# Kernel optimization log

Measured on AMD Instinct MI355X. Metric: run time of the kernel, lower is better.

The kernel has to match this reference:

```python
import jax, jax.numpy as jnp
import numpy as np

B = 4096
D = 1024
N = 100000
KS = (10000, 20000, 50000)


def _l2norm(x):
    # F.normalize(p=2, dim=1, eps=1e-12): x / max(||x||, eps)
    n = jnp.sqrt(jnp.sum(x * x, axis=1, keepdims=True))
    return x / jnp.maximum(n, 1e-12)


def setup_inputs() -> dict:
    key = jax.random.key(0)
    ks = jax.random.split(key, 16)
    inp = {}
    inp["anchor"] = jax.random.normal(ks[0], (B, D), jnp.float32)
    inp["index"] = jax.random.randint(ks[1], (B,), 0, N)
    for i, K in enumerate(KS):
        inp[f"inst2cluster{i}"] = jax.random.randint(ks[2 + i], (N,), 0, K)
        inp[f"centroids{i}"] = jax.random.normal(ks[5 + i], (K, D), jnp.float32)
        # density acts as a per-column temperature; keep it bounded away from 0
        inp[f"density{i}"] = jax.random.uniform(ks[8 + i], (K,), jnp.float32, 0.1, 1.0)
    return inp


def reference(anchor, centroids0, centroids1, centroids2,
              density0, density1, density2,
              index, inst2cluster0, inst2cluster1, inst2cluster2):
    Bn = anchor.shape[0]
    a = _l2norm(anchor)
    rows = jnp.arange(Bn)
    cols = jnp.arange(Bn - 1)
    # negatives[i, j] = sim[i, j + (j >= i)] -> row i without its diagonal entry
    neg_idx = cols[None, :] + (cols[None, :] >= rows[:, None])  # [B, B-1]

    scales = [(inst2cluster0, centroids0, density0),
              (inst2cluster1, centroids1, density1),
              (inst2cluster2, centroids2, density2)]
    n_scales = len(scales)

    loss = jnp.zeros(Bn, anchor.dtype)
    for i2c, cent, dens in scales:
        protos = _l2norm(cent)
        pos_id = i2c[index]                       # [B]
        sim = a @ protos[pos_id].T                # [B, B]
        pos = jnp.diagonal(sim)[:, None]          # [B, 1]
        neg = jnp.take_along_axis(sim, neg_idx, axis=1)  # [B, B-1]
        # torch broadcast: [B, B] / [B] divides column j by temp_proto[j]
        logits = jnp.concatenate([pos, neg], axis=1) / dens[pos_id][None, :]
        # CE with label 0, reduction='none'
        ce = jax.nn.logsumexp(logits, axis=1) - logits[:, 0]
        # faithful to the original: division by len(cluster_result) INSIDE the loop
        loss = (loss + ce) / n_scales
    return loss
```

## Files before the change

### kernel.cpp

```cpp
#include <hip/hip_runtime.h>

#define BB 4096
#define DD 1024
#define RTS (BB + 16)
#define BK 32
#define NT (DD / BK)

typedef float f32x4 __attribute__((ext_vector_type(4)));
typedef short bf16x8 __attribute__((ext_vector_type(8)));

__device__ __forceinline__ unsigned short f2bf(float f) {
  unsigned u = __float_as_uint(f);
  unsigned r = u + 0x7fffu + ((u >> 16) & 1u);
  return (unsigned short)(r >> 16);
}

__device__ __forceinline__ void async16(const void* g, void* l) {
  __builtin_amdgcn_global_load_lds(
      (const __attribute__((address_space(1))) void*)g,
      (__attribute__((address_space(3))) void*)l,
      16, 0, 0);
}

__global__ __launch_bounds__(256) void norm_anchor(const float* __restrict__ x,
                                                   unsigned short* __restrict__ y) {
  __shared__ float sred[4];
  const int row = blockIdx.x;
  const int tid = threadIdx.x;
  const float4 v = ((const float4*)(x + (size_t)row * DD))[tid];
  float ss = v.x * v.x + v.y * v.y + v.z * v.z + v.w * v.w;
#pragma unroll
  for (int off = 32; off > 0; off >>= 1) ss += __shfl_xor(ss, off, 64);
  if ((tid & 63) == 0) sred[tid >> 6] = ss;
  __syncthreads();
  const float tot = sred[0] + sred[1] + sred[2] + sred[3];
  const float inv = 1.0f / fmaxf(sqrtf(tot), 1e-12f);
  ushort4 o;
  o.x = f2bf(v.x * inv);
  o.y = f2bf(v.y * inv);
  o.z = f2bf(v.z * inv);
  o.w = f2bf(v.w * inv);
  ((ushort4*)(y + (size_t)row * DD))[tid] = o;
}

__global__ __launch_bounds__(256) void gather_norm(
    const int* __restrict__ index,
    const int* __restrict__ i2c0, const int* __restrict__ i2c1, const int* __restrict__ i2c2,
    const float* __restrict__ c0, const float* __restrict__ c1, const float* __restrict__ c2,
    const float* __restrict__ d0, const float* __restrict__ d1, const float* __restrict__ d2,
    unsigned short* __restrict__ p16, float* __restrict__ rt,
    float* __restrict__ rowacc) {
  __shared__ float sred[4];
  const int j = blockIdx.x;
  const int s = blockIdx.y;
  const int tid = threadIdx.x;
  const int* i2c = (s == 0) ? i2c0 : (s == 1) ? i2c1 : i2c2;
  const float* cent = (s == 0) ? c0 : (s == 1) ? c1 : c2;
  const float* dens = (s == 0) ? d0 : (s == 1) ? d1 : d2;
  const int pid = i2c[index[j]];
  const float4 v = ((const float4*)(cent + (size_t)pid * DD))[tid];
  float ss = v.x * v.x + v.y * v.y + v.z * v.z + v.w * v.w;
#pragma unroll
  for (int off = 32; off > 0; off >>= 1) ss += __shfl_xor(ss, off, 64);
  if ((tid & 63) == 0) sred[tid >> 6] = ss;
  __syncthreads();
  const float tot = sred[0] + sred[1] + sred[2] + sred[3];
  const float inv = 1.0f / fmaxf(sqrtf(tot), 1e-12f);
  unsigned short* out = p16 + ((size_t)s * BB + j) * DD;
  ushort4 o;
  o.x = f2bf(v.x * inv);
  o.y = f2bf(v.y * inv);
  o.z = f2bf(v.z * inv);
  o.w = f2bf(v.w * inv);
  ((ushort4*)out)[tid] = o;
  if (tid == 0) rt[(size_t)s * RTS + j] = 1.0f / dens[pid];
  if (tid == 1) rowacc[(size_t)s * BB + j] = 0.0f;
}

__global__ __launch_bounds__(512, 2) void gemm_ce_fused(const unsigned short* __restrict__ A,
                                                        const unsigned short* __restrict__ P,
                                                        const float* __restrict__ rt,
                                                        float* __restrict__ rowacc,
                                                        float* __restrict__ diag) {
  __shared__ __align__(16) unsigned short smem[4][2][8192];
  __shared__ float rsum[256][4];
  const int tid = threadIdx.x;
  const int lane = tid & 63;
  const int wave = tid >> 6;
  const int wm = wave >> 2;
  const int wn = wave & 3;
  const int m0 = blockIdx.y * 256;
  const int n0 = blockIdx.x * 256;
  const int s = blockIdx.z;
  const unsigned short* Bm = P + (size_t)s * BB * DD;
  const float* rt_s = rt + (size_t)s * RTS;

  const int row_l = lane >> 2;
  const int col_e = (((lane & 3) ^ ((row_l >> 1) & 3)) << 3);
  const int SA = wave * 2;
  const unsigned short* pA0 = A + (size_t)(m0 + SA * 16 + row_l) * DD + col_e;
  const unsigned short* pA1 = pA0 + (size_t)16 * DD;
  const unsigned short* pB0 = Bm + (size_t)(n0 + SA * 16 + row_l) * DD + col_e;
  const unsigned short* pB1 = pB0 + (size_t)16 * DD;

#pragma unroll
  for (int tt = 0; tt < 3; ++tt) {
    async16(pA0 + tt * BK, &smem[tt][0][SA * 512]);
    async16(pA1 + tt * BK, &smem[tt][0][(SA + 1) * 512]);
    async16(pB0 + tt * BK, &smem[tt][1][SA * 512]);
    async16(pB1 + tt * BK, &smem[tt][1][(SA + 1) * 512]);
  }
  const unsigned short* qA0 = pA0 + 3 * BK;
  const unsigned short* qA1 = pA1 + 3 * BK;
  const unsigned short* qB0 = pB0 + 3 * BK;
  const unsigned short* qB1 = pB1 + 3 * BK;

  const int fr = lane & 15;
  const int fq = lane >> 4;
  const int aoff = fr * 32 + ((fq ^ ((fr >> 1) & 3)) << 3);

  f32x4 acc[8][4];
#pragma unroll
  for (int mi = 0; mi < 8; ++mi)
#pragma unroll
    for (int ni = 0; ni < 4; ++ni) acc[mi][ni] = (f32x4){0.f, 0.f, 0.f, 0.f};

  for (int t = 0; t < NT; ++t) {
    const int bt = t & 3;
    const int bs = (t + 3) & 3;
    const bool stg = (t + 3 < NT);
    if (t < NT - 2)        asm volatile("s_waitcnt vmcnt(8)" ::: "memory");
    else if (t == NT - 2)  asm volatile("s_waitcnt vmcnt(4)" ::: "memory");
    else                   asm volatile("s_waitcnt vmcnt(0)" ::: "memory");
    __builtin_amdgcn_s_barrier();
    asm volatile("" ::: "memory");

    const unsigned short* la = &smem[bt][0][0];
    const unsigned short* lb = &smem[bt][1][0];

    if (stg) {
      async16(qA0, &smem[bs][0][SA * 512]);
      async16(qB0, &smem[bs][1][SA * 512]);
    }
    bf16x8 af[4], bv[4];
#pragma unroll
    for (int i = 0; i < 4; ++i) af[i] = *(const bf16x8*)&la[(wm * 8 + i) * 512 + aoff];
#pragma unroll
    for (int i = 0; i < 4; ++i) bv[i] = *(const bf16x8*)&lb[(wn * 4 + i) * 512 + aoff];
    __builtin_amdgcn_s_barrier();
    __builtin_amdgcn_s_setprio(1);
#pragma unroll
    for (int mi = 0; mi < 4; ++mi)
#pragma unroll
      for (int ni = 0; ni < 4; ++ni)
        acc[mi][ni] = __builtin_amdgcn_mfma_f32_16x16x32_bf16(af[mi], bv[ni], acc[mi][ni], 0, 0, 0);
    __builtin_amdgcn_s_setprio(0);
    __builtin_amdgcn_s_barrier();

    if (stg) {
      async16(qA1, &smem[bs][0][(SA + 1) * 512]);
      async16(qB1, &smem[bs][1][(SA + 1) * 512]);
      qA0 += BK; qA1 += BK; qB0 += BK; qB1 += BK;
    }
#pragma unroll
    for (int i = 0; i < 4; ++i) af[i] = *(const bf16x8*)&la[(wm * 8 + 4 + i) * 512 + aoff];
    __builtin_amdgcn_s_barrier();
    __builtin_amdgcn_s_setprio(1);
#pragma unroll
    for (int mi = 0; mi < 4; ++mi)
#pragma unroll
      for (int ni = 0; ni < 4; ++ni)
        acc[4 + mi][ni] = __builtin_amdgcn_mfma_f32_16x16x32_bf16(af[mi], bv[ni], acc[4 + mi][ni], 0, 0, 0);
    __builtin_amdgcn_s_setprio(0);
  }

  const int cm = fq * 4;
  const float rt0 = rt_s[0];
  float rtc[4], rtp[4];
#pragma unroll
  for (int ni = 0; ni < 4; ++ni) {
    const int col = n0 + wn * 64 + ni * 16 + fr;
    rtc[ni] = rt_s[col];
    rtp[ni] = rt_s[col + 1];
  }
#pragma unroll
  for (int mi = 0; mi < 8; ++mi) {
#pragma unroll
    for (int r = 0; r < 4; ++r) {
      const int rowi = m0 + wm * 128 + mi * 16 + cm + r;
      float esum = 0.f;
#pragma unroll
      for (int ni = 0; ni < 4; ++ni) {
        const int col = n0 + wn * 64 + ni * 16 + fr;
        const float v = acc[mi][ni][r];
        const float rr = (col == rowi) ? rt0 : ((col < rowi) ? rtp[ni] : rtc[ni]);
        const float l = v * rr;
        if (col == rowi) diag[(size_t)s * BB + rowi] = l;
        esum += __expf(l);
      }
#pragma unroll
      for (int off = 1; off < 16; off <<= 1) esum += __shfl_xor(esum, off, 64);
      if (fr == 0) rsum[wm * 128 + mi * 16 + cm + r][wn] = esum;
    }
  }
  __syncthreads();
  if (tid < 256) {
    const float v = rsum[tid][0] + rsum[tid][1] + rsum[tid][2] + rsum[tid][3];
    atomicAdd(&rowacc[(size_t)s * BB + m0 + tid], v);
  }
}

__global__ __launch_bounds__(256) void finish(const float* __restrict__ rowacc,
                                              const float* __restrict__ diag,
                                              float* __restrict__ out) {
  const int i = blockIdx.x * 256 + threadIdx.x;
  const float ce0 = logf(rowacc[i]) - diag[i];
  const float ce1 = logf(rowacc[BB + i]) - diag[BB + i];
  const float ce2 = logf(rowacc[2 * BB + i]) - diag[2 * BB + i];
  out[i] = ce0 * (1.0f / 27.0f) + ce1 * (1.0f / 9.0f) + ce2 * (1.0f / 3.0f);
}

extern "C" void kernel_launch(void* const* d_in, const int* in_sizes, int n_in,
                              void* d_out, int out_size, void* d_ws, size_t ws_size,
                              hipStream_t stream) {
  const float* anchor = (const float*)d_in[0];
  const int* index    = (const int*)d_in[1];
  const int* i2c0     = (const int*)d_in[2];
  const float* c0     = (const float*)d_in[3];
  const float* de0    = (const float*)d_in[4];
  const int* i2c1     = (const int*)d_in[5];
  const float* c1     = (const float*)d_in[6];
  const float* de1    = (const float*)d_in[7];
  const int* i2c2     = (const int*)d_in[8];
  const float* c2     = (const float*)d_in[9];
  const float* de2    = (const float*)d_in[10];

  char* ws = (char*)d_ws;
  const size_t A16_OFF = 0;
  const size_t P16_OFF = A16_OFF + (size_t)BB * DD * 2;
  const size_t RT_OFF  = P16_OFF + (size_t)3 * BB * DD * 2;
  const size_t ACC_OFF = RT_OFF + (size_t)3 * RTS * 4;
  const size_t DIA_OFF = ACC_OFF + (size_t)3 * BB * 4;

  unsigned short* a16 = (unsigned short*)(ws + A16_OFF);
  unsigned short* p16 = (unsigned short*)(ws + P16_OFF);
  float* rt     = (float*)(ws + RT_OFF);
  float* rowacc = (float*)(ws + ACC_OFF);
  float* diag   = (float*)(ws + DIA_OFF);
  float* out = (float*)d_out;

  norm_anchor<<<BB, 256, 0, stream>>>(anchor, a16);
  gather_norm<<<dim3(BB, 3), 256, 0, stream>>>(index, i2c0, i2c1, i2c2,
                                               c0, c1, c2, de0, de1, de2, p16, rt, rowacc);
  gemm_ce_fused<<<dim3(BB / 256, BB / 256, 3), 512, 0, stream>>>(a16, p16, rt, rowacc, diag);
  finish<<<BB / 256, 256, 0, stream>>>(rowacc, diag, out);
}
```

Baseline: 472.1 us.

## Simplify GEMM main loop to one barrier per k-step with interleaved A loads

Restructures the bf16 MFMA main loop. The previous version split each k-tile into two halves, using several barriers, setprio toggles and two separate async staging points. The new loop issues all four async global-to-LDS loads for the next stage right after a single barrier. It loads B fragments once and streams A fragments one row-tile at a time, interleaved with the MFMAs. This cuts barrier count and register pressure from holding A fragments. It drops the wave priority hints and the split staging that spread memory issue across the iteration, and it folds lgkmcnt(0) into the wait.

```diff
diff --git a/kernel.cpp b/kernel.cpp
--- a/kernel.cpp
+++ b/kernel.cpp
@@ -82,7 +82,7 @@
                                                         const float* __restrict__ rt,
                                                         float* __restrict__ rowacc,
                                                         float* __restrict__ diag) {
-  __shared__ __align__(16) unsigned short smem[4][2][8192];
+  __shared__ __align__(16) unsigned short smem[4][2][16][512];
   __shared__ float rsum[256][4];
   const int tid = threadIdx.x;
   const int lane = tid & 63;
@@ -98,22 +98,23 @@
   const int row_l = lane >> 2;
   const int col_e = (((lane & 3) ^ ((row_l >> 1) & 3)) << 3);
   const int SA = wave * 2;
-  const unsigned short* pA0 = A + (size_t)(m0 + SA * 16 + row_l) * DD + col_e;
-  const unsigned short* pA1 = pA0 + (size_t)16 * DD;
-  const unsigned short* pB0 = Bm + (size_t)(n0 + SA * 16 + row_l) * DD + col_e;
-  const unsigned short* pB1 = pB0 + (size_t)16 * DD;
-
-#pragma unroll
-  for (int tt = 0; tt < 3; ++tt) {
-    async16(pA0 + tt * BK, &smem[tt][0][SA * 512]);
-    async16(pA1 + tt * BK, &smem[tt][0][(SA + 1) * 512]);
-    async16(pB0 + tt * BK, &smem[tt][1][SA * 512]);
-    async16(pB1 + tt * BK, &smem[tt][1][(SA + 1) * 512]);
-  }
-  const unsigned short* qA0 = pA0 + 3 * BK;
-  const unsigned short* qA1 = pA1 + 3 * BK;
-  const unsigned short* qB0 = pB0 + 3 * BK;
-  const unsigned short* qB1 = pB1 + 3 * BK;
+  const unsigned short* gA0 = A + (size_t)(m0 + SA * 16 + row_l) * DD + col_e;
+  const unsigned short* gA1 = gA0 + (size_t)16 * DD;
+  const unsigned short* gB0 = Bm + (size_t)(n0 + SA * 16 + row_l) * DD + col_e;
+  const unsigned short* gB1 = gB0 + (size_t)16 * DD;
+
+#define STAGE4(bb)                                   \
+  do {                                               \
+    async16(gA0, &smem[bb][0][SA][0]);               \
+    async16(gA1, &smem[bb][0][SA + 1][0]);           \
+    async16(gB0, &smem[bb][1][SA][0]);               \
+    async16(gB1, &smem[bb][1][SA + 1][0]);           \
+    gA0 += BK; gA1 += BK; gB0 += BK; gB1 += BK;      \
+  } while (0)
+
+  STAGE4(0);
+  STAGE4(1);
+  STAGE4(2);
 
   const int fr = lane & 15;
   const int fq = lane >> 4;
@@ -126,53 +127,27 @@
     for (int ni = 0; ni < 4; ++ni) acc[mi][ni] = (f32x4){0.f, 0.f, 0.f, 0.f};
 
   for (int t = 0; t < NT; ++t) {
-    const int bt = t & 3;
-    const int bs = (t + 3) & 3;
-    const bool stg = (t + 3 < NT);
-    if (t < NT - 2)        asm volatile("s_waitcnt vmcnt(8)" ::: "memory");
-    else if (t == NT - 2)  asm volatile("s_waitcnt vmcnt(4)" ::: "memory");
-    else                   asm volatile("s_waitcnt vmcnt(0)" ::: "memory");
+    if (t < NT - 2)       asm volatile("s_waitcnt vmcnt(8) lgkmcnt(0)" ::: "memory");
+    else if (t == NT - 2) asm volatile("s_waitcnt vmcnt(4) lgkmcnt(0)" ::: "memory");
+    else                  asm volatile("s_waitcnt vmcnt(0) lgkmcnt(0)" ::: "memory");
     __builtin_amdgcn_s_barrier();
-    asm volatile("" ::: "memory");
-
-    const unsigned short* la = &smem[bt][0][0];
-    const unsigned short* lb = &smem[bt][1][0];
-
-    if (stg) {
-      async16(qA0, &smem[bs][0][SA * 512]);
-      async16(qB0, &smem[bs][1][SA * 512]);
+
+    const int b = t & 3;
+    if (t < NT - 3) STAGE4((t + 3) & 3);
+
+    bf16x8 bv[4];
+#pragma unroll
+    for (int ni = 0; ni < 4; ++ni)
+      bv[ni] = *(const bf16x8*)(&smem[b][1][wn * 4 + ni][0] + aoff);
+#pragma unroll
+    for (int mi = 0; mi < 8; ++mi) {
+      const bf16x8 af = *(const bf16x8*)(&smem[b][0][wm * 8 + mi][0] + aoff);
+#pragma unroll
+      for (int ni = 0; ni < 4; ++ni)
+        acc[mi][ni] = __builtin_amdgcn_mfma_f32_16x16x32_bf16(af, bv[ni], acc[mi][ni], 0, 0, 0);
     }
-    bf16x8 af[4], bv[4];
-#pragma unroll
-    for (int i = 0; i < 4; ++i) af[i] = *(const bf16x8*)&la[(wm * 8 + i) * 512 + aoff];
-#pragma unroll
-    for (int i = 0; i < 4; ++i) bv[i] = *(const bf16x8*)&lb[(wn * 4 + i) * 512 + aoff];
-    __builtin_amdgcn_s_barrier();
-    __builtin_amdgcn_s_setprio(1);
-#pragma unroll
-    for (int mi = 0; mi < 4; ++mi)
-#pragma unroll
-      for (int ni = 0; ni < 4; ++ni)
-        acc[mi][ni] = __builtin_amdgcn_mfma_f32_16x16x32_bf16(af[mi], bv[ni], acc[mi][ni], 0, 0, 0);
-    __builtin_amdgcn_s_setprio(0);
-    __builtin_amdgcn_s_barrier();
-
-    if (stg) {
-      async16(qA1, &smem[bs][0][(SA + 1) * 512]);
-      async16(qB1, &smem[bs][1][(SA + 1) * 512]);
-      qA0 += BK; qA1 += BK; qB0 += BK; qB1 += BK;
-    }
-#pragma unroll
-    for (int i = 0; i < 4; ++i) af[i] = *(const bf16x8*)&la[(wm * 8 + 4 + i) * 512 + aoff];
-    __builtin_amdgcn_s_barrier();
-    __builtin_amdgcn_s_setprio(1);
-#pragma unroll
-    for (int mi = 0; mi < 4; ++mi)
-#pragma unroll
-      for (int ni = 0; ni < 4; ++ni)
-        acc[4 + mi][ni] = __builtin_amdgcn_mfma_f32_16x16x32_bf16(af[mi], bv[ni], acc[4 + mi][ni], 0, 0, 0);
-    __builtin_amdgcn_s_setprio(0);
-  }
+  }
+#undef STAGE4
 
   const int cm = fq * 4;
   const float rt0 = rt_s[0];
```

Measured after the change: 452.6 us. -4.1%, faster.
